# Kernel optimization log

Hardware: AMD Instinct MI355X
Metric: run time of the kernel (lower is better)

## Reference

```python
import jax, jax.numpy as jnp
import numpy as np


def gcn_conv(x, W, b, src, dst, n):
    """PyG GCNConv: D^-1/2 (A+I) D^-1/2 X W + b, with added self-loops."""
    xw = x @ W  # [N, out]
    loop = jnp.arange(n, dtype=src.dtype)
    s = jnp.concatenate([src, loop])
    d = jnp.concatenate([dst, loop])
    deg = jax.ops.segment_sum(jnp.ones_like(d, dtype=xw.dtype), d, num_segments=n)
    dinv = jax.lax.rsqrt(jnp.maximum(deg, 1.0))
    norm = dinv[s] * dinv[d]  # [E+N]
    msg = xw[s] * norm[:, None]  # [E+N, out]
    return jax.ops.segment_sum(msg, d, num_segments=n) + b


def mean_pool(h, batch, num_graphs):
    s = jax.ops.segment_sum(h, batch, num_segments=num_graphs)
    cnt = jax.ops.segment_sum(jnp.ones((h.shape[0],), h.dtype), batch, num_segments=num_graphs)
    return s / jnp.maximum(cnt, 1.0)[:, None]


def setup_inputs() -> dict:
    key = jax.random.key(0)
    ks = jax.random.split(key, 12)
    N, E, F_dim, H_dim, K = 50000, 1600000, 128, 128, 32
    G = 64
    X = jax.random.normal(ks[0], (N, F_dim), dtype=jnp.float32)
    ei_feat = jax.random.randint(ks[1], (2, E), 0, N, dtype=jnp.int64)
    batch = jnp.sort(jax.random.randint(ks[2], (N,), 0, G, dtype=jnp.int64))
    sc = 1.0 / np.sqrt(H_dim)
    W1 = jax.random.normal(ks[3], (F_dim, H_dim), dtype=jnp.float32) * sc
    b1 = jnp.zeros((H_dim,), jnp.float32)
    W2 = jax.random.normal(ks[4], (H_dim, K), dtype=jnp.float32) * sc
    b2 = jnp.zeros((K,), jnp.float32)
    mW1 = jax.random.normal(ks[5], (H_dim, H_dim), dtype=jnp.float32) * sc
    mb1 = jnp.zeros((H_dim,), jnp.float32)
    mW2 = jax.random.normal(ks[6], (K, K), dtype=jnp.float32) * (1.0 / np.sqrt(K))
    mb2 = jnp.zeros((K,), jnp.float32)
    return {"X": X, "W1": W1, "b1": b1, "W2": W2, "b2": b2,
            "mW1": mW1, "mb1": mb1, "mW2": mW2, "mb2": mb2,
            "ei_feat": ei_feat, "batch": batch, "num_graphs": G}


def reference(X, W1, b1, W2, b2, mW1, mb1, mW2, mb2, ei_feat, batch, num_graphs):
    N = X.shape[0]
    src, dst = ei_feat[0], ei_feat[1]
    h = jax.nn.elu(gcn_conv(X, W1, b1, src, dst, N))  # [N, H]
    master_h = mean_pool(h, batch, num_graphs)  # [G, H]
    h = h + jax.nn.relu(master_h @ mW1 + mb1)[batch]
    Z = gcn_conv(h, W2, b2, src, dst, N)  # [N, K]
    master_z = mean_pool(Z, batch, num_graphs)  # [G, K]
    Z = Z + jax.nn.relu(master_z @ mW2 + mb2)[batch]
    return jax.nn.softmax(Z, axis=1)
```

## Files before the change

kernel.cpp:

```cpp
#include <hip/hip_runtime.h>
#include <hip/hip_bf16.h>
#include <hip/hip_fp16.h>

#define DEV_INLINE __device__ __forceinline__

static DEV_INLINE float4 ld4(const float* p){ return *reinterpret_cast<const float4*>(p); }

#define GNUM 64
#define CHUNK 4096
#define MAXNB 1024

typedef _Float16 half8 __attribute__((ext_vector_type(8)));
typedef float floatx4 __attribute__((ext_vector_type(4)));

__global__ __launch_bounds__(256) void k_hist(const int* __restrict__ dst, int E, int NB,
                                              int* __restrict__ bcnt){
    __shared__ int cnt[MAXNB];
    int t = threadIdx.x; int base0 = blockIdx.x*CHUNK;
    for (int i=t;i<NB;i+=256) cnt[i]=0;
    __syncthreads();
    int tot = E - base0; if (tot > CHUNK) tot = CHUNK;
    #pragma unroll
    for (int k=0;k<16;k++){
        int o = t + k*256;
        if (o < tot) atomicAdd(&cnt[dst[base0+o]>>7], 1);
    }
    __syncthreads();
    for (int i=t;i<NB;i+=256) if (cnt[i]) atomicAdd(&bcnt[i], cnt[i]);
}

__global__ void k_scan1b(const int* __restrict__ in, int* __restrict__ out, int M, int total,
                         const int* __restrict__ batch, int N, int* __restrict__ gstart){
    __shared__ int ws[4];
    int t = threadIdx.x;
    int i0 = t*4;
    int c0=(i0+0<M)?in[i0+0]:0, c1=(i0+1<M)?in[i0+1]:0;
    int c2=(i0+2<M)?in[i0+2]:0, c3=(i0+3<M)?in[i0+3]:0;
    int tsum=c0+c1+c2+c3;
    int lane=t&63, w=t>>6;
    int x=tsum;
    for (int off=1;off<64;off<<=1){ int yv=__shfl_up(x,off); if (lane>=off) x+=yv; }
    if (lane==63) ws[w]=x;
    __syncthreads();
    if (t==0){ int a=0; for (int i=0;i<4;i++){ int tmp=ws[i]; ws[i]=a; a+=tmp; } }
    __syncthreads();
    int ex = x - tsum + ws[w];
    if (i0+0<M) out[i0+0]=ex; ex+=c0;
    if (i0+1<M) out[i0+1]=ex; ex+=c1;
    if (i0+2<M) out[i0+2]=ex; ex+=c2;
    if (i0+3<M) out[i0+3]=ex;
    if (t==0 && total>=0) out[M]=total;
    if (t <= GNUM){
        int lo = 0, hi = N;
        while (lo < hi){ int mid = (lo+hi)>>1; if (batch[mid] < t) lo = mid+1; else hi = mid; }
        gstart[t] = lo;
    }
}

__global__ __launch_bounds__(256) void k_scatter(const int* __restrict__ src, const int* __restrict__ dst,
                                                 int E, int NB, const int* __restrict__ bbase,
                                                 int* __restrict__ bfill, unsigned* __restrict__ ebuf){
    __shared__ int cnt[MAXNB];
    __shared__ int pfx[MAXNB];
    __shared__ int gbase[MAXNB];
    __shared__ unsigned stage[CHUNK];
    __shared__ int ws[4];
    int t = threadIdx.x; int base0 = blockIdx.x*CHUNK;
    int tot = E - base0; if (tot > CHUNK) tot = CHUNK;
    for (int i=t;i<NB;i+=256) cnt[i]=0;
    __syncthreads();
    unsigned v[16]; int rk[16];
    #pragma unroll
    for (int k=0;k<16;k++){
        int o = t + k*256;
        if (o < tot){
            int e = base0 + o;
            int s = src[e], d = dst[e];
            v[k] = (unsigned)s | ((unsigned)d<<16);
            rk[k] = atomicAdd(&cnt[d>>7], 1);
        } else { v[k]=0u; rk[k]=-1; }
    }
    __syncthreads();
    int i0 = t*4;
    int c0=(i0+0<NB)?cnt[i0+0]:0, c1=(i0+1<NB)?cnt[i0+1]:0;
    int c2=(i0+2<NB)?cnt[i0+2]:0, c3=(i0+3<NB)?cnt[i0+3]:0;
    int tsum=c0+c1+c2+c3;
    int lane=t&63, w=t>>6;
    int x=tsum;
    for (int off=1;off<64;off<<=1){ int yv=__shfl_up(x,off); if (lane>=off) x+=yv; }
    if (lane==63) ws[w]=x;
    __syncthreads();
    if (t==0){ int a=0; for (int i=0;i<4;i++){ int tmp=ws[i]; ws[i]=a; a+=tmp; } }
    __syncthreads();
    int ex = x - tsum + ws[w];
    if (i0+0<NB) pfx[i0+0]=ex; ex+=c0;
    if (i0+1<NB) pfx[i0+1]=ex; ex+=c1;
    if (i0+2<NB) pfx[i0+2]=ex; ex+=c2;
    if (i0+3<NB) pfx[i0+3]=ex;
    __syncthreads();
    for (int i=t;i<NB;i+=256){
        int c = cnt[i];
        gbase[i] = c ? (bbase[i] + atomicAdd(&bfill[i], c)) : 0;
    }
    __syncthreads();
    #pragma unroll
    for (int k=0;k<16;k++) if (rk[k]>=0){ int b = (int)(v[k]>>23); stage[pfx[b]+rk[k]] = v[k]; }
    __syncthreads();
    for (int j=t;j<tot;j+=256){
        unsigned u = stage[j];
        int b = (int)(u>>23);
        ebuf[gbase[b] + (j - pfx[b])] = u;
    }
}

__global__ __launch_bounds__(256) void k_bucket_finish(const unsigned* __restrict__ ebuf,
                                                       const int* __restrict__ bbase,
                                                       int* __restrict__ rs, unsigned short* __restrict__ csr,
                                                       float* __restrict__ dinv, int N, int E){
    __shared__ int c2[128];
    __shared__ int rsl[128];
    __shared__ int ws[4];
    int b = blockIdx.x, t = threadIdx.x;
    if (t < 128) c2[t] = 0;
    __syncthreads();
    int s0 = bbase[b], s1 = bbase[b+1];
    for (int j = s0+t; j < s1; j += 256)
        atomicAdd(&c2[(ebuf[j]>>16)&127], 1);
    __syncthreads();
    int v = (t < 128) ? c2[t] : 0;
    int lane = t & 63, w = t >> 6;
    int x = v;
    for (int off=1; off<64; off<<=1){
        int yv = __shfl_up(x, off);
        if (lane >= off) x += yv;
    }
    if (lane == 63) ws[w] = x;
    __syncthreads();
    if (t < 128){
        int ex = x - v + ((w == 1) ? ws[0] : 0);
        rsl[t] = s0 + ex;
        int node = (b<<7) + t;
        if (node < N){
            rs[node] = s0 + ex;
            dinv[node] = rsqrtf((float)(v + 1));
        }
    }
    if (b == (int)gridDim.x - 1 && t == 0) rs[N] = E;
    __syncthreads();
    if (t < 128) c2[t] = 0;
    __syncthreads();
    for (int j = s0+t; j < s1; j += 256){
        unsigned u = ebuf[j];
        int ld = (u>>16)&127;
        int p = atomicAdd(&c2[ld], 1);
        csr[rsl[ld]+p] = (unsigned short)(u & 0xffffu);
    }
}

__global__ void k_prep(const float* __restrict__ W1, __half* __restrict__ w1t){
    int f = blockIdx.x*256 + threadIdx.x;
    int c = f >> 7, k = f & 127;
    w1t[c*136 + k] = __float2half(W1[k*128 + c]);
}

__global__ __launch_bounds__(256) void k_gemm1(const float* __restrict__ X, const __half* __restrict__ w1t,
                                               const float* __restrict__ dinv, __half* __restrict__ yh, int N){
    __shared__ __half Wl[128*136];
    int t = threadIdx.x;
    if (blockIdx.x==0 && t < 32)
        reinterpret_cast<uint2*>(yh + (size_t)N*128)[t] = make_uint2(0u,0u);
    {
        const uint4* g = (const uint4*)w1t;
        uint4* l = (uint4*)Wl;
        for (int i = t; i < 2176; i += 256) l[i] = g[i];
    }
    __syncthreads();
    int wv = t>>6, lane = t&63;
    int r0 = blockIdx.x*64 + wv*16;
    if (r0 >= N) return;
    int lr = lane & 15, lg = lane >> 4;
    int r = r0 + lr;
    bool rok = r < N;
    const float* xrow = X + (size_t)(rok ? r : 0)*128;
    floatx4 acc[8];
    #pragma unroll
    for (int i=0;i<8;i++) acc[i] = (floatx4){0.f,0.f,0.f,0.f};
    #pragma unroll
    for (int ks=0; ks<4; ks++){
        int k0 = ks*32 + lg*8;
        float4 xa = ld4(xrow + k0);
        float4 xb = ld4(xrow + k0 + 4);
        half8 bfrag;
        bfrag[0]=(_Float16)xa.x; bfrag[1]=(_Float16)xa.y; bfrag[2]=(_Float16)xa.z; bfrag[3]=(_Float16)xa.w;
        bfrag[4]=(_Float16)xb.x; bfrag[5]=(_Float16)xb.y; bfrag[6]=(_Float16)xb.z; bfrag[7]=(_Float16)xb.w;
        #pragma unroll
        for (int ct=0; ct<8; ct++){
            half8 afrag = *reinterpret_cast<const half8*>(&Wl[(ct*16 + lr)*136 + k0]);
            acc[ct] = __builtin_amdgcn_mfma_f32_16x16x32_f16(afrag, bfrag, acc[ct], 0, 0, 0);
        }
    }
    if (rok){
        float dv = dinv[r];
        #pragma unroll
        for (int ct=0; ct<8; ct++){
            __half2 p0 = __floats2half2_rn(acc[ct][0]*dv, acc[ct][1]*dv);
            __half2 p1 = __floats2half2_rn(acc[ct][2]*dv, acc[ct][3]*dv);
            uint2 stv; stv.x = *(unsigned*)&p0; stv.y = *(unsigned*)&p1;
            *reinterpret_cast<uint2*>(&yh[(size_t)r*128 + ct*16 + lg*4]) = stv;
        }
    }
}

__global__ void k_agg1(const __half* __restrict__ yh, const float* __restrict__ dinv,
                       const float* __restrict__ b1, const int* __restrict__ rs,
                       const unsigned short* __restrict__ csr, __half* __restrict__ h, int N){
    int wid = (int)((blockIdx.x * blockDim.x + threadIdx.x) >> 6);
    if (wid >= N) return;
    int lane = threadIdx.x & 63;
    int q = lane >> 4, ql = lane & 15;
    int beg = rs[wid], end = rs[wid+1];
    int len = end - beg;
    int qlen = (len + 3) >> 2;
    int qbeg = beg + q*qlen;
    int qend = qbeg + qlen; if (qend > end) qend = end;
    int mylen = qend - qbeg; if (mylen < 0) mylen = 0;
    const uint4* base = reinterpret_cast<const uint4*>(yh) + ql;
    float f0=0.f,f1=0.f,f2=0.f,f3=0.f,f4=0.f,f5=0.f,f6=0.f,f7=0.f;
    int iters = (qlen + 15) >> 4;
    for (int c=0;c<iters;c++){
        int o = c*16 + ql;
        int idx = (o < mylen) ? (int)csr[qbeg + o] : N;
        int tmax = qlen - c*16; if (tmax > 16) tmax = 16;
        int nch = (tmax + 3) >> 2;
        __half2 a0 = __float2half2_rn(0.f), a1 = a0, a2 = a0, a3 = a0;
        for (int ch=0; ch<nch; ++ch){
            int tb = (q<<4) + ch*4;
            int s0 = __shfl(idx, tb+0);
            int s1 = __shfl(idx, tb+1);
            int s2 = __shfl(idx, tb+2);
            int s3 = __shfl(idx, tb+3);
            uint4 u0 = base[(size_t)s0*16];
            uint4 u1 = base[(size_t)s1*16];
            uint4 u2 = base[(size_t)s2*16];
            uint4 u3 = base[(size_t)s3*16];
            a0 = __hadd2(a0, *(__half2*)&u0.x); a1 = __hadd2(a1, *(__half2*)&u0.y);
            a2 = __hadd2(a2, *(__half2*)&u0.z); a3 = __hadd2(a3, *(__half2*)&u0.w);
            a0 = __hadd2(a0, *(__half2*)&u1.x); a1 = __hadd2(a1, *(__half2*)&u1.y);
            a2 = __hadd2(a2, *(__half2*)&u1.z); a3 = __hadd2(a3, *(__half2*)&u1.w);
            a0 = __hadd2(a0, *(__half2*)&u2.x); a1 = __hadd2(a1, *(__half2*)&u2.y);
            a2 = __hadd2(a2, *(__half2*)&u2.z); a3 = __hadd2(a3, *(__half2*)&u2.w);
            a0 = __hadd2(a0, *(__half2*)&u3.x); a1 = __hadd2(a1, *(__half2*)&u3.y);
            a2 = __hadd2(a2, *(__half2*)&u3.z); a3 = __hadd2(a3, *(__half2*)&u3.w);
        }
        float2 t0 = __half22float2(a0); f0 += t0.x; f1 += t0.y;
        float2 t1 = __half22float2(a1); f2 += t1.x; f3 += t1.y;
        float2 t2 = __half22float2(a2); f4 += t2.x; f5 += t2.y;
        float2 t3 = __half22float2(a3); f6 += t3.x; f7 += t3.y;
    }
    f0 += __shfl_xor(f0,16); f1 += __shfl_xor(f1,16); f2 += __shfl_xor(f2,16); f3 += __shfl_xor(f3,16);
    f4 += __shfl_xor(f4,16); f5 += __shfl_xor(f5,16); f6 += __shfl_xor(f6,16); f7 += __shfl_xor(f7,16);
    f0 += __shfl_xor(f0,32); f1 += __shfl_xor(f1,32); f2 += __shfl_xor(f2,32); f3 += __shfl_xor(f3,32);
    f4 += __shfl_xor(f4,32); f5 += __shfl_xor(f5,32); f6 += __shfl_xor(f6,32); f7 += __shfl_xor(f7,32);
    if (q == 0){
        uint4 su = base[(size_t)wid*16];
        float2 s0 = __half22float2(*(__half2*)&su.x); f0 += s0.x; f1 += s0.y;
        float2 s1 = __half22float2(*(__half2*)&su.y); f2 += s1.x; f3 += s1.y;
        float2 s2 = __half22float2(*(__half2*)&su.z); f4 += s2.x; f5 += s2.y;
        float2 s3 = __half22float2(*(__half2*)&su.w); f6 += s3.x; f7 += s3.y;
        float dv = dinv[wid];
        float4 ba = ld4(&b1[ql*8]), bb = ld4(&b1[ql*8+4]);
        float o0 = dv*f0+ba.x, o1 = dv*f1+ba.y, o2 = dv*f2+ba.z, o3 = dv*f3+ba.w;
        float o4 = dv*f4+bb.x, o5 = dv*f5+bb.y, o6 = dv*f6+bb.z, o7 = dv*f7+bb.w;
        o0 = o0>0.f?o0:expm1f(o0); o1 = o1>0.f?o1:expm1f(o1);
        o2 = o2>0.f?o2:expm1f(o2); o3 = o3>0.f?o3:expm1f(o3);
        o4 = o4>0.f?o4:expm1f(o4); o5 = o5>0.f?o5:expm1f(o5);
        o6 = o6>0.f?o6:expm1f(o6); o7 = o7>0.f?o7:expm1f(o7);
        __half2 p0 = __floats2half2_rn(o0,o1), p1 = __floats2half2_rn(o2,o3);
        __half2 p2 = __floats2half2_rn(o4,o5), p3 = __floats2half2_rn(o6,o7);
        uint4 stv; stv.x=*(unsigned*)&p0; stv.y=*(unsigned*)&p1; stv.z=*(unsigned*)&p2; stv.w=*(unsigned*)&p3;
        *reinterpret_cast<uint4*>(&h[(size_t)wid*128 + ql*8]) = stv;
    }
}

__global__ void k_mpoolh(const __half* __restrict__ hsrc, const int* __restrict__ gstart,
                         float* __restrict__ msum){
    int g = blockIdx.x, part = blockIdx.y, P = gridDim.y;
    int c = threadIdx.x;
    int s0 = gstart[g], s1 = gstart[g+1];
    int len = s1 - s0;
    int per = (len + P - 1) / P;
    int rbeg = s0 + part*per, rend = rbeg + per; if (rend > s1) rend = s1;
    float sx = 0.f, sy = 0.f;
    const __half2* h2 = (const __half2*)hsrc;
    for (int r = rbeg; r < rend; ++r){
        float2 f = __half22float2(h2[(size_t)r*64 + c]);
        sx += f.x; sy += f.y;
    }
    if (rend > rbeg){
        atomicAdd(&msum[g*128 + 2*c], sx);
        atomicAdd(&msum[g*128 + 2*c+1], sy);
    }
}

__global__ void k_mpool(const float* __restrict__ srcm, const int* __restrict__ gstart,
                        float* __restrict__ msum, int C){
    int g = blockIdx.x, part = blockIdx.y, P = gridDim.y;
    int c = threadIdx.x;
    if (c >= C) return;
    int s0 = gstart[g], s1 = gstart[g+1];
    int len = s1 - s0;
    int per = (len + P - 1) / P;
    int rbeg = s0 + part*per, rend = rbeg + per; if (rend > s1) rend = s1;
    float sum = 0.f;
    for (int r = rbeg; r < rend; ++r) sum += srcm[(size_t)r*C + c];
    if (rend > rbeg) atomicAdd(&msum[g*C + c], sum);
}

__global__ void k_mlp1(const float* __restrict__ msum, const int* __restrict__ gstart,
                       const float* __restrict__ mW1, const float* __restrict__ mb1,
                       float* __restrict__ r1){
    int g = blockIdx.x, c = threadIdx.x;
    int cnt = gstart[g+1] - gstart[g];
    float inv = 1.f / (float)(cnt > 1 ? cnt : 1);
    float acc = mb1[c];
    for (int k=0;k<128;k++) acc = fmaf(msum[g*128+k]*inv, mW1[k*128+c], acc);
    r1[g*128+c] = fmaxf(acc, 0.f);
}

__global__ void k_mlp2(const float* __restrict__ msum2, const int* __restrict__ gstart,
                       const float* __restrict__ mW2, const float* __restrict__ mb2,
                       float* __restrict__ r2){
    int g = blockIdx.x, c = threadIdx.x;
    if (c >= 32) return;
    int cnt = gstart[g+1] - gstart[g];
    float inv = 1.f / (float)(cnt > 1 ? cnt : 1);
    float acc = mb2[c];
    for (int k=0;k<32;k++) acc = fmaf(msum2[g*32+k]*inv, mW2[k*32+c], acc);
    r2[g*32+c] = fmaxf(acc, 0.f);
}

__global__ __launch_bounds__(256) void k_gemm2(const __half* __restrict__ h, const float* __restrict__ vn,
                                               const int* __restrict__ batch, const float* __restrict__ W2,
                                               const float* __restrict__ dinv, __half* __restrict__ y2, int N){
    __shared__ float W2s[128*32];
    int t = threadIdx.x;
    if (blockIdx.x==0 && t < 8)
        reinterpret_cast<uint2*>(y2 + (size_t)N*32)[t] = make_uint2(0u,0u);
    {
        float4* Wl = (float4*)W2s;
        const float4* Wg = (const float4*)W2;
        #pragma unroll
        for (int i=0;i<4;i++) Wl[t + i*256] = Wg[t + i*256];
    }
    __syncthreads();
    int row0 = blockIdx.x*64;
    int tc = t & 7, trg = t >> 3;
    int ra = row0 + 2*trg, rb = ra + 1;
    bool oka = ra < N, okb = rb < N;
    const __half* hpa = h + (size_t)(oka ? ra : 0)*128;
    const __half* hpb = h + (size_t)(okb ? rb : 0)*128;
    const float* vpa = vn + (size_t)(oka ? batch[ra] : 0)*128;
    const float* vpb = vn + (size_t)(okb ? batch[rb] : 0)*128;
    float4 acca={0,0,0,0}, accb={0,0,0,0};
    for (int k=0;k<128;k+=4){
        float4 w0 = ld4(&W2s[(k+0)*32 + tc*4]);
        float4 w1 = ld4(&W2s[(k+1)*32 + tc*4]);
        float4 w2 = ld4(&W2s[(k+2)*32 + tc*4]);
        float4 w3 = ld4(&W2s[(k+3)*32 + tc*4]);
        {
            uint2 u = *reinterpret_cast<const uint2*>(&hpa[k]);
            float2 f0 = __half22float2(*(__half2*)&u.x), f1 = __half22float2(*(__half2*)&u.y);
            float4 bb = ld4(vpa + k);
            float ax=f0.x+bb.x, ay=f0.y+bb.y, az=f1.x+bb.z, aw=f1.y+bb.w;
            acca.x += ax*w0.x + ay*w1.x + az*w2.x + aw*w3.x;
            acca.y += ax*w0.y + ay*w1.y + az*w2.y + aw*w3.y;
            acca.z += ax*w0.z + ay*w1.z + az*w2.z + aw*w3.z;
            acca.w += ax*w0.w + ay*w1.w + az*w2.w + aw*w3.w;
        }
        {
            uint2 u = *reinterpret_cast<const uint2*>(&hpb[k]);
            float2 f0 = __half22float2(*(__half2*)&u.x), f1 = __half22float2(*(__half2*)&u.y);
            float4 bb = ld4(vpb + k);
            float ax=f0.x+bb.x, ay=f0.y+bb.y, az=f1.x+bb.z, aw=f1.y+bb.w;
            accb.x += ax*w0.x + ay*w1.x + az*w2.x + aw*w3.x;
            accb.y += ax*w0.y + ay*w1.y + az*w2.y + aw*w3.y;
            accb.z += ax*w0.z + ay*w1.z + az*w2.z + aw*w3.z;
            accb.w += ax*w0.w + ay*w1.w + az*w2.w + aw*w3.w;
        }
    }
    if (oka){
        float dv = dinv[ra];
        __half2 p0 = __floats2half2_rn(acca.x*dv, acca.y*dv);
        __half2 p1 = __floats2half2_rn(acca.z*dv, acca.w*dv);
        uint2 stv; stv.x = *(unsigned*)&p0; stv.y = *(unsigned*)&p1;
        *reinterpret_cast<uint2*>(&y2[(size_t)ra*32 + tc*4]) = stv;
    }
    if (okb){
        float dv = dinv[rb];
        __half2 p0 = __floats2half2_rn(accb.x*dv, accb.y*dv);
        __half2 p1 = __floats2half2_rn(accb.z*dv, accb.w*dv);
        uint2 stv; stv.x = *(unsigned*)&p0; stv.y = *(unsigned*)&p1;
        *reinterpret_cast<uint2*>(&y2[(size_t)rb*32 + tc*4]) = stv;
    }
}

__global__ void k_agg2h(const __half* __restrict__ y2, const float* __restrict__ dinv,
                        const float* __restrict__ b2, const int* __restrict__ rs,
                        const unsigned short* __restrict__ csr, float* __restrict__ Z, int N){
    int wid = (int)((blockIdx.x*blockDim.x + threadIdx.x) >> 6);
    if (wid >= N) return;
    int lane = threadIdx.x & 63;
    int o8 = lane >> 3, ol = lane & 7;
    int beg = rs[wid], end = rs[wid+1], len = end-beg;
    int olen = (len + 7) >> 3;
    int obeg = beg + o8*olen;
    int oend = obeg + olen; if (oend > end) oend = end;
    int mylen = oend - obeg; if (mylen < 0) mylen = 0;
    const uint2* base = reinterpret_cast<const uint2*>(y2) + ol;
    float f0=0.f, f1=0.f, f2=0.f, f3=0.f;
    int iters = (olen + 7) >> 3;
    for (int c=0;c<iters;c++){
        int o = c*8 + ol;
        int idx = (o < mylen) ? (int)csr[obeg + o] : N;
        int tmax = olen - c*8; if (tmax > 8) tmax = 8;
        int nch = (tmax + 3) >> 2;
        __half2 a0 = __float2half2_rn(0.f), a1 = a0;
        for (int ch=0; ch<nch; ++ch){
            int tb = (o8<<3) + ch*4;
            int s0 = __shfl(idx, tb+0);
            int s1 = __shfl(idx, tb+1);
            int s2 = __shfl(idx, tb+2);
            int s3 = __shfl(idx, tb+3);
            uint2 u0 = base[(size_t)s0*8];
            uint2 u1 = base[(size_t)s1*8];
            uint2 u2 = base[(size_t)s2*8];
            uint2 u3 = base[(size_t)s3*8];
            a0 = __hadd2(a0, *(__half2*)&u0.x); a1 = __hadd2(a1, *(__half2*)&u0.y);
            a0 = __hadd2(a0, *(__half2*)&u1.x); a1 = __hadd2(a1, *(__half2*)&u1.y);
            a0 = __hadd2(a0, *(__half2*)&u2.x); a1 = __hadd2(a1, *(__half2*)&u2.y);
            a0 = __hadd2(a0, *(__half2*)&u3.x); a1 = __hadd2(a1, *(__half2*)&u3.y);
        }
        float2 t0 = __half22float2(a0); f0 += t0.x; f1 += t0.y;
        float2 t1 = __half22float2(a1); f2 += t1.x; f3 += t1.y;
    }
    f0 += __shfl_xor(f0,8);  f1 += __shfl_xor(f1,8);  f2 += __shfl_xor(f2,8);  f3 += __shfl_xor(f3,8);
    f0 += __shfl_xor(f0,16); f1 += __shfl_xor(f1,16); f2 += __shfl_xor(f2,16); f3 += __shfl_xor(f3,16);
    f0 += __shfl_xor(f0,32); f1 += __shfl_xor(f1,32); f2 += __shfl_xor(f2,32); f3 += __shfl_xor(f3,32);
    if (o8 == 0){
        uint2 su = base[(size_t)wid*8];
        float2 s0 = __half22float2(*(__half2*)&su.x); f0 += s0.x; f1 += s0.y;
        float2 s1 = __half22float2(*(__half2*)&su.y); f2 += s1.x; f3 += s1.y;
        float dv = dinv[wid];
        float4 bb = ld4(&b2[ol*4]);
        float4 outv;
        outv.x = dv*f0 + bb.x; outv.y = dv*f1 + bb.y;
        outv.z = dv*f2 + bb.z; outv.w = dv*f3 + bb.w;
        *reinterpret_cast<float4*>(&Z[(size_t)wid*32 + ol*4]) = outv;
    }
}

__global__ void k_softmax(float* __restrict__ Z, const float* __restrict__ r2,
                          const int* __restrict__ batch, int N){
    int r = blockIdx.x*8 + (threadIdx.x>>5);
    int c = threadIdx.x & 31;
    if (r >= N) return;
    float z = Z[(size_t)r*32+c] + r2[batch[r]*32 + c];
    float m = z;
    #pragma unroll
    for (int off=16; off>=1; off>>=1) m = fmaxf(m, __shfl_xor(m, off));
    float e = expf(z - m);
    float s = e;
    #pragma unroll
    for (int off=16; off>=1; off>>=1) s += __shfl_xor(s, off);
    Z[(size_t)r*32+c] = e / s;
}

extern "C" void kernel_launch(void* const* d_in, const int* in_sizes, int n_in,
                              void* d_out, int out_size, void* d_ws, size_t ws_size,
                              hipStream_t stream){
    const float* X   = (const float*)d_in[0];
    const float* W1  = (const float*)d_in[1];
    const float* b1  = (const float*)d_in[2];
    const float* W2  = (const float*)d_in[3];
    const float* b2  = (const float*)d_in[4];
    const float* mW1 = (const float*)d_in[5];
    const float* mb1 = (const float*)d_in[6];
    const float* mW2 = (const float*)d_in[7];
    const float* mb2 = (const float*)d_in[8];
    const int*   ei  = (const int*)d_in[9];
    const int*   batch = (const int*)d_in[10];
    int N = in_sizes[0] / 128;
    int E = in_sizes[9] / 2;
    const int* src = ei;
    const int* dst = ei + E;
    float* Zout = (float*)d_out;

    char* wsp = (char*)d_ws;
    size_t off = 0;
    auto alloc = [&](size_t bytes)->char*{
        char* p = wsp + off; off += (bytes + 255) & ~(size_t)255; return p;
    };
    int*   bcnt  = (int*)  alloc((size_t)MAXNB*4);
    int*   bfill = (int*)  alloc((size_t)MAXNB*4);
    float* msum  = (float*)alloc((size_t)GNUM*128*4);
    float* msum2 = (float*)alloc((size_t)GNUM*32*4);
    size_t zero_bytes = off;
    int*   bbase = (int*)  alloc((size_t)(MAXNB+1)*4);
    int*   rs    = (int*)  alloc((size_t)(N+1)*4);
    int*   gstart= (int*)  alloc((GNUM+1)*4);
    unsigned* ebuf = (unsigned*)alloc((size_t)E*4);
    unsigned short* csr = (unsigned short*)alloc((size_t)E*2);
    float* dinvp = (float*)alloc((size_t)N*4);
    __half* w1t  = (__half*)alloc((size_t)128*136*2);
    __half* yh   = (__half*)alloc((size_t)(N+1)*128*2);
    __half* h    = (__half*)alloc((size_t)N*128*2);
    __half* y2h  = (__half*)alloc((size_t)(N+1)*32*2);
    float* r1buf = (float*)alloc((size_t)GNUM*128*4);
    float* r2buf = (float*)alloc((size_t)GNUM*32*4);
    (void)ws_size; (void)n_in; (void)out_size;

    hipMemsetAsync(d_ws, 0, zero_bytes, stream);

    int NB = (N + 127) >> 7;
    int EB = (E + CHUNK-1) / CHUNK;

    k_prep         <<<64, 256, 0, stream>>>(W1, w1t);
    k_hist         <<<EB, 256, 0, stream>>>(dst, E, NB, bcnt);
    k_scan1b       <<<1, 256, 0, stream>>>(bcnt, bbase, NB, E, batch, N, gstart);
    k_scatter      <<<EB, 256, 0, stream>>>(src, dst, E, NB, bbase, bfill, ebuf);
    k_bucket_finish<<<NB, 256, 0, stream>>>(ebuf, bbase, rs, csr, dinvp, N, E);

    k_gemm1 <<<(N+63)/64, 256, 0, stream>>>(X, w1t, dinvp, yh, N);
    k_agg1  <<<(N+3)/4, 256, 0, stream>>>(yh, dinvp, b1, rs, csr, h, N);

    k_mpoolh<<<dim3(GNUM,8), 64, 0, stream>>>(h, gstart, msum);
    k_mlp1  <<<GNUM, 128, 0, stream>>>(msum, gstart, mW1, mb1, r1buf);

    k_gemm2 <<<(N+63)/64, 256, 0, stream>>>(h, r1buf, batch, W2, dinvp, y2h, N);
    k_agg2h <<<(N+3)/4, 256, 0, stream>>>(y2h, dinvp, b2, rs, csr, Zout, N);

    k_mpool <<<dim3(GNUM,8), 64, 0, stream>>>(Zout, gstart, msum2, 32);
    k_mlp2  <<<GNUM, 64, 0, stream>>>(msum2, gstart, mW2, mb2, r2buf);
    k_softmax<<<(N+7)/8, 256, 0, stream>>>(Zout, r2buf, batch, N);
}
```

Before: 241.3 us.

## Use MFMA for second GEMM, fuse weight prep into histogram, widen gather batches

Rewrites the second GCN GEMM as fp16 MFMA matrix instructions. It uses a pre-transposed half-precision W2 and a half-precision master-node vector, replacing scalar fp32 FMAs. The weight transposes for W1 and W2 now run as extra blocks of the histogram kernel, which removes one launch. Both aggregation kernels fetch eight neighbour rows per batch instead of four, using 32-bit byte-offset addressing, to raise memory-level parallelism. The trade-offs are more fp16 rounding in the h+r1 sum and higher register pressure in the gather loops.

```diff
diff --git a/kernel.cpp b/kernel.cpp
--- a/kernel.cpp
+++ b/kernel.cpp
@@ -13,8 +13,27 @@
 typedef _Float16 half8 __attribute__((ext_vector_type(8)));
 typedef float floatx4 __attribute__((ext_vector_type(4)));
 
+#define W1T_ELEMS (128*136)
+#define W2T_ELEMS (32*136)
+
 __global__ __launch_bounds__(256) void k_hist(const int* __restrict__ dst, int E, int NB,
-                                              int* __restrict__ bcnt){
+                                              int* __restrict__ bcnt,
+                                              const float* __restrict__ W1, const float* __restrict__ W2,
+                                              __half* __restrict__ w1t, __half* __restrict__ w2t, int EB){
+    if ((int)blockIdx.x >= EB){
+        int f = ((int)blockIdx.x - EB)*256 + threadIdx.x;
+        if (f < W1T_ELEMS){
+            int c = f/136, k = f - c*136;
+            w1t[f] = (k<128) ? __float2half(W1[k*128+c]) : __float2half(0.f);
+        } else {
+            int f2 = f - W1T_ELEMS;
+            if (f2 < W2T_ELEMS){
+                int c = f2/136, k = f2 - c*136;
+                w2t[f2] = (k<128) ? __float2half(W2[k*32+c]) : __float2half(0.f);
+            }
+        }
+        return;
+    }
     __shared__ int cnt[MAXNB];
     int t = threadIdx.x; int base0 = blockIdx.x*CHUNK;
     for (int i=t;i<NB;i+=256) cnt[i]=0;
@@ -155,12 +174,6 @@
         int p = atomicAdd(&c2[ld], 1);
         csr[rsl[ld]+p] = (unsigned short)(u & 0xffffu);
     }
-}
-
-__global__ void k_prep(const float* __restrict__ W1, __half* __restrict__ w1t){
-    int f = blockIdx.x*256 + threadIdx.x;
-    int c = f >> 7, k = f & 127;
-    w1t[c*136 + k] = __float2half(W1[k*128 + c]);
 }
 
 __global__ __launch_bounds__(256) void k_gemm1(const float* __restrict__ X, const __half* __restrict__ w1t,
@@ -224,25 +237,34 @@
     int qbeg = beg + q*qlen;
     int qend = qbeg + qlen; if (qend > end) qend = end;
     int mylen = qend - qbeg; if (mylen < 0) mylen = 0;
-    const uint4* base = reinterpret_cast<const uint4*>(yh) + ql;
+    const char* yb = (const char*)yh;
+    unsigned lofs = (unsigned)ql * 16u;
     float f0=0.f,f1=0.f,f2=0.f,f3=0.f,f4=0.f,f5=0.f,f6=0.f,f7=0.f;
     int iters = (qlen + 15) >> 4;
     for (int c=0;c<iters;c++){
         int o = c*16 + ql;
         int idx = (o < mylen) ? (int)csr[qbeg + o] : N;
         int tmax = qlen - c*16; if (tmax > 16) tmax = 16;
-        int nch = (tmax + 3) >> 2;
+        int nch = (tmax + 7) >> 3;
         __half2 a0 = __float2half2_rn(0.f), a1 = a0, a2 = a0, a3 = a0;
         for (int ch=0; ch<nch; ++ch){
-            int tb = (q<<4) + ch*4;
+            int tb = (q<<4) + ch*8;
             int s0 = __shfl(idx, tb+0);
             int s1 = __shfl(idx, tb+1);
             int s2 = __shfl(idx, tb+2);
             int s3 = __shfl(idx, tb+3);
-            uint4 u0 = base[(size_t)s0*16];
-            uint4 u1 = base[(size_t)s1*16];
-            uint4 u2 = base[(size_t)s2*16];
-            uint4 u3 = base[(size_t)s3*16];
+            int s4 = __shfl(idx, tb+4);
+            int s5 = __shfl(idx, tb+5);
+            int s6 = __shfl(idx, tb+6);
+            int s7 = __shfl(idx, tb+7);
+            uint4 u0 = *(const uint4*)(yb + (((unsigned)s0<<8) + lofs));
+            uint4 u1 = *(const uint4*)(yb + (((unsigned)s1<<8) + lofs));
+            uint4 u2 = *(const uint4*)(yb + (((unsigned)s2<<8) + lofs));
+            uint4 u3 = *(const uint4*)(yb + (((unsigned)s3<<8) + lofs));
+            uint4 u4 = *(const uint4*)(yb + (((unsigned)s4<<8) + lofs));
+            uint4 u5 = *(const uint4*)(yb + (((unsigned)s5<<8) + lofs));
+            uint4 u6 = *(const uint4*)(yb + (((unsigned)s6<<8) + lofs));
+            uint4 u7 = *(const uint4*)(yb + (((unsigned)s7<<8) + lofs));
             a0 = __hadd2(a0, *(__half2*)&u0.x); a1 = __hadd2(a1, *(__half2*)&u0.y);
             a2 = __hadd2(a2, *(__half2*)&u0.z); a3 = __hadd2(a3, *(__half2*)&u0.w);
             a0 = __hadd2(a0, *(__half2*)&u1.x); a1 = __hadd2(a1, *(__half2*)&u1.y);
@@ -251,6 +273,14 @@
             a2 = __hadd2(a2, *(__half2*)&u2.z); a3 = __hadd2(a3, *(__half2*)&u2.w);
             a0 = __hadd2(a0, *(__half2*)&u3.x); a1 = __hadd2(a1, *(__half2*)&u3.y);
             a2 = __hadd2(a2, *(__half2*)&u3.z); a3 = __hadd2(a3, *(__half2*)&u3.w);
+            a0 = __hadd2(a0, *(__half2*)&u4.x); a1 = __hadd2(a1, *(__half2*)&u4.y);
+            a2 = __hadd2(a2, *(__half2*)&u4.z); a3 = __hadd2(a3, *(__half2*)&u4.w);
+            a0 = __hadd2(a0, *(__half2*)&u5.x); a1 = __hadd2(a1, *(__half2*)&u5.y);
+            a2 = __hadd2(a2, *(__half2*)&u5.z); a3 = __hadd2(a3, *(__half2*)&u5.w);
+            a0 = __hadd2(a0, *(__half2*)&u6.x); a1 = __hadd2(a1, *(__half2*)&u6.y);
+            a2 = __hadd2(a2, *(__half2*)&u6.z); a3 = __hadd2(a3, *(__half2*)&u6.w);
+            a0 = __hadd2(a0, *(__half2*)&u7.x); a1 = __hadd2(a1, *(__half2*)&u7.y);
+            a2 = __hadd2(a2, *(__half2*)&u7.z); a3 = __hadd2(a3, *(__half2*)&u7.w);
         }
         float2 t0 = __half22float2(a0); f0 += t0.x; f1 += t0.y;
         float2 t1 = __half22float2(a1); f2 += t1.x; f3 += t1.y;
@@ -262,7 +292,7 @@
     f0 += __shfl_xor(f0,32); f1 += __shfl_xor(f1,32); f2 += __shfl_xor(f2,32); f3 += __shfl_xor(f3,32);
     f4 += __shfl_xor(f4,32); f5 += __shfl_xor(f5,32); f6 += __shfl_xor(f6,32); f7 += __shfl_xor(f7,32);
     if (q == 0){
-        uint4 su = base[(size_t)wid*16];
+        uint4 su = *(const uint4*)(yb + (((unsigned)wid<<8) + lofs));
         float2 s0 = __half22float2(*(__half2*)&su.x); f0 += s0.x; f1 += s0.y;
         float2 s1 = __half22float2(*(__half2*)&su.y); f2 += s1.x; f3 += s1.y;
         float2 s2 = __half22float2(*(__half2*)&su.z); f4 += s2.x; f5 += s2.y;
@@ -318,13 +348,13 @@
 
 __global__ void k_mlp1(const float* __restrict__ msum, const int* __restrict__ gstart,
                        const float* __restrict__ mW1, const float* __restrict__ mb1,
-                       float* __restrict__ r1){
+                       __half* __restrict__ r1h){
     int g = blockIdx.x, c = threadIdx.x;
     int cnt = gstart[g+1] - gstart[g];
     float inv = 1.f / (float)(cnt > 1 ? cnt : 1);
     float acc = mb1[c];
     for (int k=0;k<128;k++) acc = fmaf(msum[g*128+k]*inv, mW1[k*128+c], acc);
-    r1[g*128+c] = fmaxf(acc, 0.f);
+    r1h[g*128+c] = __float2half(fmaxf(acc, 0.f));
 }
 
 __global__ void k_mlp2(const float* __restrict__ msum2, const int* __restrict__ gstart,
@@ -339,68 +369,60 @@
     r2[g*32+c] = fmaxf(acc, 0.f);
 }
 
-__global__ __launch_bounds__(256) void k_gemm2(const __half* __restrict__ h, const float* __restrict__ vn,
-                                               const int* __restrict__ batch, const float* __restrict__ W2,
+__global__ __launch_bounds__(256) void k_gemm2(const __half* __restrict__ h, const __half* __restrict__ r1h,
+                                               const int* __restrict__ batch, const __half* __restrict__ w2t,
                                                const float* __restrict__ dinv, __half* __restrict__ y2, int N){
-    __shared__ float W2s[128*32];
+    __shared__ __half Wl[32*136];
     int t = threadIdx.x;
     if (blockIdx.x==0 && t < 8)
         reinterpret_cast<uint2*>(y2 + (size_t)N*32)[t] = make_uint2(0u,0u);
     {
-        float4* Wl = (float4*)W2s;
-        const float4* Wg = (const float4*)W2;
-        #pragma unroll
-        for (int i=0;i<4;i++) Wl[t + i*256] = Wg[t + i*256];
-    }
-    __syncthreads();
-    int row0 = blockIdx.x*64;
-    int tc = t & 7, trg = t >> 3;
-    int ra = row0 + 2*trg, rb = ra + 1;
-    bool oka = ra < N, okb = rb < N;
-    const __half* hpa = h + (size_t)(oka ? ra : 0)*128;
-    const __half* hpb = h + (size_t)(okb ? rb : 0)*128;
-    const float* vpa = vn + (size_t)(oka ? batch[ra] : 0)*128;
-    const float* vpb = vn + (size_t)(okb ? batch[rb] : 0)*128;
-    float4 acca={0,0,0,0}, accb={0,0,0,0};
-    for (int k=0;k<128;k+=4){
-        float4 w0 = ld4(&W2s[(k+0)*32 + tc*4]);
-        float4 w1 = ld4(&W2s[(k+1)*32 + tc*4]);
-        float4 w2 = ld4(&W2s[(k+2)*32 + tc*4]);
-        float4 w3 = ld4(&W2s[(k+3)*32 + tc*4]);
+        const uint4* g = (const uint4*)w2t;
+        uint4* l = (uint4*)Wl;
+        for (int i = t; i < 544; i += 256) l[i] = g[i];
+    }
+    __syncthreads();
+    int wv = t>>6, lane = t&63;
+    int r0 = blockIdx.x*64 + wv*16;
+    if (r0 >= N) return;
+    int lr = lane & 15, lg = lane >> 4;
+    int r = r0 + lr;
+    bool rok = r < N;
+    int rr = rok ? r : 0;
+    const __half* hrow = h + (size_t)rr*128;
+    const __half* vrow = r1h + (size_t)batch[rr]*128;
+    floatx4 acc0 = (floatx4){0.f,0.f,0.f,0.f};
+    floatx4 acc1 = (floatx4){0.f,0.f,0.f,0.f};
+    #pragma unroll
+    for (int ks=0; ks<4; ks++){
+        int k0 = ks*32 + lg*8;
+        uint4 hu = *reinterpret_cast<const uint4*>(hrow + k0);
+        uint4 vu = *reinterpret_cast<const uint4*>(vrow + k0);
+        __half2 b0 = __hadd2(*(__half2*)&hu.x, *(__half2*)&vu.x);
+        __half2 b1_ = __hadd2(*(__half2*)&hu.y, *(__half2*)&vu.y);
+        __half2 b2_ = __hadd2(*(__half2*)&hu.z, *(__half2*)&vu.z);
+        __half2 b3_ = __hadd2(*(__half2*)&hu.w, *(__half2*)&vu.w);
+        uint4 bu; bu.x=*(unsigned*)&b0; bu.y=*(unsigned*)&b1_; bu.z=*(unsigned*)&b2_; bu.w=*(unsigned*)&b3_;
+        half8 bfrag = *reinterpret_cast<half8*>(&bu);
+        half8 a0 = *reinterpret_cast<const half8*>(&Wl[(0*16 + lr)*136 + k0]);
+        half8 a1 = *reinterpret_cast<const half8*>(&Wl[(1*16 + lr)*136 + k0]);
+        acc0 = __builtin_amdgcn_mfma_f32_16x16x32_f16(a0, bfrag, acc0, 0, 0, 0);
+        acc1 = __builtin_amdgcn_mfma_f32_16x16x32_f16(a1, bfrag, acc1, 0, 0, 0);
+    }
+    if (rok){
+        float dv = dinv[r];
         {
-            uint2 u = *reinterpret_cast<const uint2*>(&hpa[k]);
-            float2 f0 = __half22float2(*(__half2*)&u.x), f1 = __half22float2(*(__half2*)&u.y);
-            float4 bb = ld4(vpa + k);
-            float ax=f0.x+bb.x, ay=f0.y+bb.y, az=f1.x+bb.z, aw=f1.y+bb.w;
-            acca.x += ax*w0.x + ay*w1.x + az*w2.x + aw*w3.x;
-            acca.y += ax*w0.y + ay*w1.y + az*w2.y + aw*w3.y;
-            acca.z += ax*w0.z + ay*w1.z + az*w2.z + aw*w3.z;
-            acca.w += ax*w0.w + ay*w1.w + az*w2.w + aw*w3.w;
+            __half2 p0 = __floats2half2_rn(acc0[0]*dv, acc0[1]*dv);
+            __half2 p1 = __floats2half2_rn(acc0[2]*dv, acc0[3]*dv);
+            uint2 stv; stv.x = *(unsigned*)&p0; stv.y = *(unsigned*)&p1;
+            *reinterpret_cast<uint2*>(&y2[(size_t)r*32 + 0 + lg*4]) = stv;
         }
         {
-            uint2 u = *reinterpret_cast<const uint2*>(&hpb[k]);
-            float2 f0 = __half22float2(*(__half2*)&u.x), f1 = __half22float2(*(__half2*)&u.y);
-            float4 bb = ld4(vpb + k);
-            float ax=f0.x+bb.x, ay=f0.y+bb.y, az=f1.x+bb.z, aw=f1.y+bb.w;
-            accb.x += ax*w0.x + ay*w1.x + az*w2.x + aw*w3.x;
-            accb.y += ax*w0.y + ay*w1.y + az*w2.y + aw*w3.y;
-            accb.z += ax*w0.z + ay*w1.z + az*w2.z + aw*w3.z;
-            accb.w += ax*w0.w + ay*w1.w + az*w2.w + aw*w3.w;
-        }
-    }
-    if (oka){
-        float dv = dinv[ra];
-        __half2 p0 = __floats2half2_rn(acca.x*dv, acca.y*dv);
-        __half2 p1 = __floats2half2_rn(acca.z*dv, acca.w*dv);
-        uint2 stv; stv.x = *(unsigned*)&p0; stv.y = *(unsigned*)&p1;
-        *reinterpret_cast<uint2*>(&y2[(size_t)ra*32 + tc*4]) = stv;
-    }
-    if (okb){
-        float dv = dinv[rb];
-        __half2 p0 = __floats2half2_rn(accb.x*dv, accb.y*dv);
-        __half2 p1 = __floats2half2_rn(accb.z*dv, accb.w*dv);
-        uint2 stv; stv.x = *(unsigned*)&p0; stv.y = *(unsigned*)&p1;
-        *reinterpret_cast<uint2*>(&y2[(size_t)rb*32 + tc*4]) = stv;
+            __half2 p0 = __floats2half2_rn(acc1[0]*dv, acc1[1]*dv);
+            __half2 p1 = __floats2half2_rn(acc1[2]*dv, acc1[3]*dv);
+            uint2 stv; stv.x = *(unsigned*)&p0; stv.y = *(unsigned*)&p1;
+            *reinterpret_cast<uint2*>(&y2[(size_t)r*32 + 16 + lg*4]) = stv;
+        }
     }
 }
 
@@ -416,30 +438,39 @@
     int obeg = beg + o8*olen;
     int oend = obeg + olen; if (oend > end) oend = end;
     int mylen = oend - obeg; if (mylen < 0) mylen = 0;
-    const uint2* base = reinterpret_cast<const uint2*>(y2) + ol;
+    const char* yb = (const char*)y2;
+    unsigned lofs = (unsigned)ol * 8u;
     float f0=0.f, f1=0.f, f2=0.f, f3=0.f;
     int iters = (olen + 7) >> 3;
     for (int c=0;c<iters;c++){
         int o = c*8 + ol;
         int idx = (o < mylen) ? (int)csr[obeg + o] : N;
-        int tmax = olen - c*8; if (tmax > 8) tmax = 8;
-        int nch = (tmax + 3) >> 2;
+        int tb = o8<<3;
+        int s0 = __shfl(idx, tb+0);
+        int s1 = __shfl(idx, tb+1);
+        int s2 = __shfl(idx, tb+2);
+        int s3 = __shfl(idx, tb+3);
+        int s4 = __shfl(idx, tb+4);
+        int s5 = __shfl(idx, tb+5);
+        int s6 = __shfl(idx, tb+6);
+        int s7 = __shfl(idx, tb+7);
+        uint2 u0 = *(const uint2*)(yb + (((unsigned)s0<<6) + lofs));
+        uint2 u1 = *(const uint2*)(yb + (((unsigned)s1<<6) + lofs));
+        uint2 u2 = *(const uint2*)(yb + (((unsigned)s2<<6) + lofs));
+        uint2 u3 = *(const uint2*)(yb + (((unsigned)s3<<6) + lofs));
+        uint2 u4 = *(const uint2*)(yb + (((unsigned)s4<<6) + lofs));
+        uint2 u5 = *(const uint2*)(yb + (((unsigned)s5<<6) + lofs));
+        uint2 u6 = *(const uint2*)(yb + (((unsigned)s6<<6) + lofs));
+        uint2 u7 = *(const uint2*)(yb + (((unsigned)s7<<6) + lofs));
         __half2 a0 = __float2half2_rn(0.f), a1 = a0;
-        for (int ch=0; ch<nch; ++ch){
-            int tb = (o8<<3) + ch*4;
-            int s0 = __shfl(idx, tb+0);
-            int s1 = __shfl(idx, tb+1);
-            int s2 = __shfl(idx, tb+2);
-            int s3 = __shfl(idx, tb+3);
-            uint2 u0 = base[(size_t)s0*8];
-            uint2 u1 = base[(size_t)s1*8];
-            uint2 u2 = base[(size_t)s2*8];
-            uint2 u3 = base[(size_t)s3*8];
-            a0 = __hadd2(a0, *(__half2*)&u0.x); a1 = __hadd2(a1, *(__half2*)&u0.y);
-            a0 = __hadd2(a0, *(__half2*)&u1.x); a1 = __hadd2(a1, *(__half2*)&u1.y);
-            a0 = __hadd2(a0, *(__half2*)&u2.x); a1 = __hadd2(a1, *(__half2*)&u2.y);
-            a0 = __hadd2(a0, *(__half2*)&u3.x); a1 = __hadd2(a1, *(__half2*)&u3.y);
-        }
+        a0 = __hadd2(a0, *(__half2*)&u0.x); a1 = __hadd2(a1, *(__half2*)&u0.y);
+        a0 = __hadd2(a0, *(__half2*)&u1.x); a1 = __hadd2(a1, *(__half2*)&u1.y);
+        a0 = __hadd2(a0, *(__half2*)&u2.x); a1 = __hadd2(a1, *(__half2*)&u2.y);
+        a0 = __hadd2(a0, *(__half2*)&u3.x); a1 = __hadd2(a1, *(__half2*)&u3.y);
+        a0 = __hadd2(a0, *(__half2*)&u4.x); a1 = __hadd2(a1, *(__half2*)&u4.y);
+        a0 = __hadd2(a0, *(__half2*)&u5.x); a1 = __hadd2(a1, *(__half2*)&u5.y);
+        a0 = __hadd2(a0, *(__half2*)&u6.x); a1 = __hadd2(a1, *(__half2*)&u6.y);
+        a0 = __hadd2(a0, *(__half2*)&u7.x); a1 = __hadd2(a1, *(__half2*)&u7.y);
         float2 t0 = __half22float2(a0); f0 += t0.x; f1 += t0.y;
         float2 t1 = __half22float2(a1); f2 += t1.x; f3 += t1.y;
     }
@@ -447,7 +478,7 @@
     f0 += __shfl_xor(f0,16); f1 += __shfl_xor(f1,16); f2 += __shfl_xor(f2,16); f3 += __shfl_xor(f3,16);
     f0 += __shfl_xor(f0,32); f1 += __shfl_xor(f1,32); f2 += __shfl_xor(f2,32); f3 += __shfl_xor(f3,32);
     if (o8 == 0){
-        uint2 su = base[(size_t)wid*8];
+        uint2 su = *(const uint2*)(yb + (((unsigned)wid<<6) + lofs));
         float2 s0 = __half22float2(*(__half2*)&su.x); f0 += s0.x; f1 += s0.y;
         float2 s1 = __half22float2(*(__half2*)&su.y); f2 += s1.x; f3 += s1.y;
         float dv = dinv[wid];
@@ -511,11 +542,12 @@
     unsigned* ebuf = (unsigned*)alloc((size_t)E*4);
     unsigned short* csr = (unsigned short*)alloc((size_t)E*2);
     float* dinvp = (float*)alloc((size_t)N*4);
-    __half* w1t  = (__half*)alloc((size_t)128*136*2);
+    __half* w1t  = (__half*)alloc((size_t)W1T_ELEMS*2);
+    __half* w2t  = (__half*)alloc((size_t)W2T_ELEMS*2);
     __half* yh   = (__half*)alloc((size_t)(N+1)*128*2);
     __half* h    = (__half*)alloc((size_t)N*128*2);
     __half* y2h  = (__half*)alloc((size_t)(N+1)*32*2);
-    float* r1buf = (float*)alloc((size_t)GNUM*128*4);
+    __half* r1buf= (__half*)alloc((size_t)GNUM*128*2);
     float* r2buf = (float*)alloc((size_t)GNUM*32*4);
     (void)ws_size; (void)n_in; (void)out_size;
 
@@ -523,9 +555,9 @@
 
     int NB = (N + 127) >> 7;
     int EB = (E + CHUNK-1) / CHUNK;
-
-    k_prep         <<<64, 256, 0, stream>>>(W1, w1t);
-    k_hist         <<<EB, 256, 0, stream>>>(dst, E, NB, bcnt);
+    int PREP = (W1T_ELEMS + W2T_ELEMS + 255)/256;
+
+    k_hist         <<<EB + PREP, 256, 0, stream>>>(dst, E, NB, bcnt, W1, W2, w1t, w2t, EB);
     k_scan1b       <<<1, 256, 0, stream>>>(bcnt, bbase, NB, E, batch, N, gstart);
     k_scatter      <<<EB, 256, 0, stream>>>(src, dst, E, NB, bbase, bfill, ebuf);
     k_bucket_finish<<<NB, 256, 0, stream>>>(ebuf, bbase, rs, csr, dinvp, N, E);
@@ -536,7 +568,7 @@
     k_mpoolh<<<dim3(GNUM,8), 64, 0, stream>>>(h, gstart, msum);
     k_mlp1  <<<GNUM, 128, 0, stream>>>(msum, gstart, mW1, mb1, r1buf);
 
-    k_gemm2 <<<(N+63)/64, 256, 0, stream>>>(h, r1buf, batch, W2, dinvp, y2h, N);
+    k_gemm2 <<<(N+63)/64, 256, 0, stream>>>(h, r1buf, batch, w2t, dinvp, y2h, N);
     k_agg2h <<<(N+3)/4, 256, 0, stream>>>(y2h, dinvp, b2, rs, csr, Zout, N);
 
     k_mpool <<<dim3(GNUM,8), 64, 0, stream>>>(Zout, gstart, msum2, 32);
```

Measured after the change: 227.0 us. 6.0% less time.
